# Performance work log

Hardware: AMD Instinct MI355X
Metric: run time of the kernel (lower is better)

The kernel has to match this reference:

```python
import jax, jax.numpy as jnp
import numpy as np

N = 1024
IN_FEATURES = 128
N_HEADS = 8
N_HIDDEN = 16  # out_features // n_heads = 128 // 8
NEG_SLOPE = 0.2


def setup_inputs() -> dict:
    key = jax.random.key(0)
    k1, k2, k3, k4, k5 = jax.random.split(key, 5)
    h = jax.random.normal(k1, (N, IN_FEATURES), dtype=jnp.float32)
    adj_mat = jax.random.randint(k2, (N, N, 1), 0, 2, dtype=jnp.int32)
    s = jax.random.normal(k3, (N, N, 1), dtype=jnp.float32)
    # linear: nn.Linear(in_features, n_hidden*n_heads, bias=False) -> weight [128, 128]
    W = jax.random.normal(k4, (N_HEADS * N_HIDDEN, IN_FEATURES), dtype=jnp.float32) * 0.1
    # attn: nn.Linear(2*n_hidden, 1, bias=False) -> weight [1, 32]; stored flat [32]
    attn_w = jax.random.normal(k5, (2 * N_HIDDEN,), dtype=jnp.float32) * 0.1
    return {"h": h, "adj_mat": adj_mat, "s": s, "W": W, "attn_w": attn_w}


def reference(h, adj_mat, s, W, attn_w):
    n_nodes = h.shape[0]
    # g: [N, heads, hidden]
    g = (h @ W.T).reshape(n_nodes, N_HEADS, N_HIDDEN)
    # attn(cat(g_i, g_j)) = a_src . g_i + a_dst . g_j  (linear decomposes over concat)
    a_src = attn_w[:N_HIDDEN]
    a_dst = attn_w[N_HIDDEN:]
    src = jnp.einsum('ihf,f->ih', g, a_src)  # [N, heads]
    dst = jnp.einsum('jhf,f->jh', g, a_dst)  # [N, heads]
    e = jax.nn.leaky_relu(src[:, None, :] + dst[None, :, :], NEG_SLOPE)  # [N, N, heads]
    mask = adj_mat == 0  # [N, N, 1] broadcasts over heads
    neg_inf = jnp.array(-jnp.inf, dtype=e.dtype)
    e = jnp.where(mask, neg_inf, e)
    s_masked = jnp.where(mask, neg_inf, s)  # [N, N, 1]
    a = jax.nn.softmax(e, axis=1)               # [N, N, heads]
    s_prime = jax.nn.softmax(s_masked, axis=1)  # [N, N, 1]
    # NOTE: original applies a third softmax to (a + s_prime) WITHOUT re-masking,
    # so non-edge entries (value 0) get nonzero weight exp(0)/Z — replicated faithfully.
    new_attention = jax.nn.softmax(a + s_prime, axis=1)  # [N, N, heads]
    # dropout is identity in eval mode
    attn_res = jnp.einsum('ijh,jhf->ihf', new_attention, g)  # [N, heads, hidden]
    return attn_res.reshape(n_nodes, N_HEADS * N_HIDDEN)
```

## Files before the change

### kernel.cpp

```cpp
#include <hip/hip_runtime.h>

#define NNODES 1024
#define NHEADS 8
#define NHID 16
#define DIM 128
#define NEG_SLOPE 0.2f

__global__ __launch_bounds__(128) void proj_kernel(
    const float* __restrict__ h, const float* __restrict__ W,
    const float* __restrict__ attn_w,
    float* __restrict__ g, float* __restrict__ srcv, float* __restrict__ dstv)
{
    const int i = blockIdx.x;
    const int o = threadIdx.x;
    __shared__ float hs[DIM];
    hs[o] = h[(size_t)i * DIM + o];
    __syncthreads();
    const float4* hv = (const float4*)hs;
    const float4* wv = (const float4*)(W + (size_t)o * DIM);
    float acc = 0.f;
#pragma unroll
    for (int k = 0; k < DIM / 4; k++) {
        float4 a = hv[k]; float4 b = wv[k];
        acc = fmaf(a.x, b.x, fmaf(a.y, b.y, fmaf(a.z, b.z, fmaf(a.w, b.w, acc))));
    }
    g[(size_t)i * DIM + o] = acc;
    const int f  = o & (NHID - 1);
    const int hd = o >> 4;
    float sv = acc * attn_w[f];
    float dv = acc * attn_w[NHID + f];
#pragma unroll
    for (int off = 8; off > 0; off >>= 1) {
        sv += __shfl_xor(sv, off, 64);
        dv += __shfl_xor(dv, off, 64);
    }
    if (f == 0) { srcv[i * NHEADS + hd] = sv; dstv[i * NHEADS + hd] = dv; }
}

__global__ __launch_bounds__(256, 2) void fused_kernel(
    const int* __restrict__ adj, const float* __restrict__ s,
    const float* __restrict__ g, const float* __restrict__ srcv,
    const float* __restrict__ dstv, float* __restrict__ out)
{
    const int i0   = blockIdx.x * 2;
    const int tid  = threadIdx.x;
    const int lane = tid & 63;
    const int wv   = tid >> 6;
    const int hA   = tid & 7;
    const int jsA  = tid >> 3;
    const int qB   = tid & 3;
    const int hB   = (tid >> 2) & 7;
    const int jsB  = tid >> 5;

    __shared__ float evL[2][NNODES];
    __shared__ float dstL[NNODES * NHEADS];
    __shared__ float sh_src[2][NHEADS];
    __shared__ float zeA[4][NHEADS][2];
    __shared__ float zsA[4][2];
    __shared__ float statE[2][NHEADS];
    __shared__ float statS[2];
    __shared__ float redO[4][2][NHEADS][4][4];
    __shared__ float ztA[4][2][NHEADS];

    float zs[2] = {0.f, 0.f};
#pragma unroll
    for (int r = 0; r < 2; r++) {
        const int4   a  = ((const int4*)  adj)[(size_t)(i0 + r) * (NNODES/4) + tid];
        const float4 sv = ((const float4*)s  )[(size_t)(i0 + r) * (NNODES/4) + tid];
        float4 e4;
        e4.x = a.x ? __expf(sv.x) : 0.f;
        e4.y = a.y ? __expf(sv.y) : 0.f;
        e4.z = a.z ? __expf(sv.z) : 0.f;
        e4.w = a.w ? __expf(sv.w) : 0.f;
        ((float4*)evL[r])[tid] = e4;
        zs[r] += e4.x + e4.y + e4.z + e4.w;
    }
    {
        const float4* dv4 = (const float4*)dstv;
        float4* dl4 = (float4*)dstL;
#pragma unroll
        for (int k = 0; k < 8; k++) dl4[k * 256 + tid] = dv4[k * 256 + tid];
        if (tid < 16) sh_src[tid >> 3][tid & 7] =
            srcv[(size_t)(i0 + (tid >> 3)) * NHEADS + (tid & 7)];
    }
    __syncthreads();

    float ze[2] = {0.f, 0.f};
    {
        const float sHA[2] = { sh_src[0][hA], sh_src[1][hA] };
#pragma unroll 4
        for (int t = 0; t < 32; t++) {
            const int j = t * 32 + jsA;
            const float d = dstL[j * NHEADS + hA];
#pragma unroll
            for (int r = 0; r < 2; r++) {
                float e = sHA[r] + d;
                e = e > 0.f ? e : NEG_SLOPE * e;
                const float x = __expf(e);
                ze[r] += (evL[r][j] != 0.f) ? x : 0.f;
            }
        }
    }
#pragma unroll
    for (int off = 8; off <= 32; off <<= 1)
#pragma unroll
        for (int r = 0; r < 2; r++) ze[r] += __shfl_xor(ze[r], off, 64);
#pragma unroll
    for (int off = 1; off <= 32; off <<= 1)
#pragma unroll
        for (int r = 0; r < 2; r++) zs[r] += __shfl_xor(zs[r], off, 64);
    if (lane < NHEADS) { zeA[wv][lane][0] = ze[0]; zeA[wv][lane][1] = ze[1]; }
    if (lane == 0)     { zsA[wv][0] = zs[0]; zsA[wv][1] = zs[1]; }
    __syncthreads();
    if (tid < 16) {
        const int hh = tid & 7, rr = tid >> 3;
        statE[rr][hh] = 1.f / (zeA[0][hh][rr] + zeA[1][hh][rr] +
                               zeA[2][hh][rr] + zeA[3][hh][rr]);
    } else if (tid < 18) {
        const int rr = tid - 16;
        statS[rr] = 1.f / (zsA[0][rr] + zsA[1][rr] + zsA[2][rr] + zsA[3][rr]);
    }
    __syncthreads();

    const float ize[2] = { statE[0][hB], statE[1][hB] };
    const float izs[2] = { statS[0],     statS[1]     };
    const float sHB[2] = { sh_src[0][hB], sh_src[1][hB] };
    const int   base   = lane & ~3;

    float acc[2][4] = {{0.f,0.f,0.f,0.f},{0.f,0.f,0.f,0.f}};
    float zt[2] = {0.f, 0.f};
    const float4* g4 = (const float4*)g;

#pragma unroll 2
    for (int tg = 0; tg < 32; tg++) {
        const int jw = (tg * 4 + qB) * 8 + jsB;
        const float d = dstL[jw * NHEADS + hB];
        float w[2];
#pragma unroll
        for (int r = 0; r < 2; r++) {
            float e = sHB[r] + d;
            e = e > 0.f ? e : NEG_SLOPE * e;
            const float x  = __expf(e);
            const float ev = evL[r][jw];
            const float arg = (ev != 0.f) ? fmaf(x, ize[r], ev * izs[r]) : 0.f;
            w[r] = __expf(arg);
            zt[r] += w[r];
        }
#pragma unroll
        for (int k = 0; k < 4; k++) {
            const int j = (tg * 4 + k) * 8 + jsB;
            const float4 gv = g4[(size_t)j * 32 + hB * 4 + qB];
            const float w0 = __shfl(w[0], base + k, 64);
            const float w1 = __shfl(w[1], base + k, 64);
            acc[0][0] = fmaf(w0, gv.x, acc[0][0]);
            acc[0][1] = fmaf(w0, gv.y, acc[0][1]);
            acc[0][2] = fmaf(w0, gv.z, acc[0][2]);
            acc[0][3] = fmaf(w0, gv.w, acc[0][3]);
            acc[1][0] = fmaf(w1, gv.x, acc[1][0]);
            acc[1][1] = fmaf(w1, gv.y, acc[1][1]);
            acc[1][2] = fmaf(w1, gv.z, acc[1][2]);
            acc[1][3] = fmaf(w1, gv.w, acc[1][3]);
        }
    }

#pragma unroll
    for (int r = 0; r < 2; r++)
#pragma unroll
        for (int m = 0; m < 4; m++) acc[r][m] += __shfl_xor(acc[r][m], 32, 64);
#pragma unroll
    for (int r = 0; r < 2; r++) {
        zt[r] += __shfl_xor(zt[r], 1, 64);
        zt[r] += __shfl_xor(zt[r], 2, 64);
        zt[r] += __shfl_xor(zt[r], 32, 64);
    }
    if (lane < 32) {
#pragma unroll
        for (int r = 0; r < 2; r++)
            *(float4*)&redO[wv][r][hB][qB][0] =
                make_float4(acc[r][0], acc[r][1], acc[r][2], acc[r][3]);
        if ((lane & 3) == 0) { ztA[wv][0][hB] = zt[0]; ztA[wv][1][hB] = zt[1]; }
    }
    __syncthreads();
    {
        const int rr = tid >> 7;
        const int hf = tid & 127;
        const int oh = hf >> 4;
        const int qq = (hf >> 2) & 3;
        const int mm = hf & 3;
        const float v  = redO[0][rr][oh][qq][mm] + redO[1][rr][oh][qq][mm] +
                         redO[2][rr][oh][qq][mm] + redO[3][rr][oh][qq][mm];
        const float zq = ztA[0][rr][oh] + ztA[1][rr][oh] +
                         ztA[2][rr][oh] + ztA[3][rr][oh];
        out[(size_t)(i0 + rr) * DIM + hf] = v / zq;
    }
}

extern "C" void kernel_launch(void* const* d_in, const int* in_sizes, int n_in,
                              void* d_out, int out_size, void* d_ws, size_t ws_size,
                              hipStream_t stream) {
    const float* h      = (const float*)d_in[0];
    const int*   adj    = (const int*)  d_in[1];
    const float* s      = (const float*)d_in[2];
    const float* W      = (const float*)d_in[3];
    const float* attn_w = (const float*)d_in[4];
    float* out = (float*)d_out;

    float* g    = (float*)d_ws;
    float* srcv = g    + (size_t)NNODES * DIM;
    float* dstv = srcv + (size_t)NNODES * NHEADS;

    proj_kernel <<<NNODES, DIM, 0, stream>>>(h, W, attn_w, g, srcv, dstv);
    fused_kernel<<<NNODES / 2, 256, 0, stream>>>(adj, s, g, srcv, dstv, out);
}
```

Before: 87.43 us.

## Store projected features in fp16 and cache first-pass exponentials in LDS

The projected feature matrix g is now written in half precision and read as packed half2 in the aggregation loop, which halves its memory traffic. The first pass stores exp(leaky_relu) values for both rows as half2 in a padded LDS buffer, so the second pass skips recomputing them, and dst values are read straight from global memory instead of being staged in LDS. The aggregation thread mapping changes so each thread owns 8 features and no cross-lane weight shuffles are needed. This cuts exp work and bandwidth but adds fp16 rounding error on g and the attention logits.

```diff
diff --git a/kernel.cpp b/kernel.cpp
--- a/kernel.cpp
+++ b/kernel.cpp
@@ -1,15 +1,19 @@
 #include <hip/hip_runtime.h>
+#include <hip/hip_fp16.h>
 
 #define NNODES 1024
 #define NHEADS 8
 #define NHID 16
 #define DIM 128
 #define NEG_SLOPE 0.2f
+#define XSTRIDE 36
+
+union F2H { float f; __half2 h; };
 
 __global__ __launch_bounds__(128) void proj_kernel(
     const float* __restrict__ h, const float* __restrict__ W,
     const float* __restrict__ attn_w,
-    float* __restrict__ g, float* __restrict__ srcv, float* __restrict__ dstv)
+    __half* __restrict__ gh, float* __restrict__ srcv, float* __restrict__ dstv)
 {
     const int i = blockIdx.x;
     const int o = threadIdx.x;
@@ -24,7 +28,7 @@
         float4 a = hv[k]; float4 b = wv[k];
         acc = fmaf(a.x, b.x, fmaf(a.y, b.y, fmaf(a.z, b.z, fmaf(a.w, b.w, acc))));
     }
-    g[(size_t)i * DIM + o] = acc;
+    gh[(size_t)i * DIM + o] = __float2half_rn(acc);
     const int f  = o & (NHID - 1);
     const int hd = o >> 4;
     float sv = acc * attn_w[f];
@@ -39,30 +43,25 @@
 
 __global__ __launch_bounds__(256, 2) void fused_kernel(
     const int* __restrict__ adj, const float* __restrict__ s,
-    const float* __restrict__ g, const float* __restrict__ srcv,
+    const __half* __restrict__ gh, const float* __restrict__ srcv,
     const float* __restrict__ dstv, float* __restrict__ out)
 {
     const int i0   = blockIdx.x * 2;
     const int tid  = threadIdx.x;
     const int lane = tid & 63;
     const int wv   = tid >> 6;
-    const int hA   = tid & 7;
-    const int jsA  = tid >> 3;
-    const int qB   = tid & 3;
-    const int hB   = (tid >> 2) & 7;
-    const int jsB  = tid >> 5;
 
     __shared__ float evL[2][NNODES];
-    __shared__ float dstL[NNODES * NHEADS];
+    __shared__ float xLf[256 * XSTRIDE];
     __shared__ float sh_src[2][NHEADS];
     __shared__ float zeA[4][NHEADS][2];
     __shared__ float zsA[4][2];
     __shared__ float statE[2][NHEADS];
     __shared__ float statS[2];
-    __shared__ float redO[4][2][NHEADS][4][4];
+    __shared__ float redO[4][2][NHEADS][2][8];
     __shared__ float ztA[4][2][NHEADS];
 
-    float zs[2] = {0.f, 0.f};
+    float zs0 = 0.f, zs1 = 0.f;
 #pragma unroll
     for (int r = 0; r < 2; r++) {
         const int4   a  = ((const int4*)  adj)[(size_t)(i0 + r) * (NNODES/4) + tid];
@@ -73,44 +72,55 @@
         e4.z = a.z ? __expf(sv.z) : 0.f;
         e4.w = a.w ? __expf(sv.w) : 0.f;
         ((float4*)evL[r])[tid] = e4;
-        zs[r] += e4.x + e4.y + e4.z + e4.w;
-    }
-    {
-        const float4* dv4 = (const float4*)dstv;
-        float4* dl4 = (float4*)dstL;
-#pragma unroll
-        for (int k = 0; k < 8; k++) dl4[k * 256 + tid] = dv4[k * 256 + tid];
-        if (tid < 16) sh_src[tid >> 3][tid & 7] =
-            srcv[(size_t)(i0 + (tid >> 3)) * NHEADS + (tid & 7)];
-    }
-    __syncthreads();
-
-    float ze[2] = {0.f, 0.f};
-    {
-        const float sHA[2] = { sh_src[0][hA], sh_src[1][hA] };
-#pragma unroll 4
-        for (int t = 0; t < 32; t++) {
-            const int j = t * 32 + jsA;
-            const float d = dstL[j * NHEADS + hA];
-#pragma unroll
-            for (int r = 0; r < 2; r++) {
-                float e = sHA[r] + d;
-                e = e > 0.f ? e : NEG_SLOPE * e;
-                const float x = __expf(e);
-                ze[r] += (evL[r][j] != 0.f) ? x : 0.f;
-            }
-        }
-    }
-#pragma unroll
-    for (int off = 8; off <= 32; off <<= 1)
-#pragma unroll
-        for (int r = 0; r < 2; r++) ze[r] += __shfl_xor(ze[r], off, 64);
-#pragma unroll
-    for (int off = 1; off <= 32; off <<= 1)
-#pragma unroll
-        for (int r = 0; r < 2; r++) zs[r] += __shfl_xor(zs[r], off, 64);
-    if (lane < NHEADS) { zeA[wv][lane][0] = ze[0]; zeA[wv][lane][1] = ze[1]; }
-    if (lane == 0)     { zsA[wv][0] = zs[0]; zsA[wv][1] = zs[1]; }
+        const float t = e4.x + e4.y + e4.z + e4.w;
+        if (r == 0) zs0 += t; else zs1 += t;
+    }
+    if (tid < 16) sh_src[tid >> 3][tid & 7] =
+        srcv[(size_t)(i0 + (tid >> 3)) * NHEADS + (tid & 7)];
+    __syncthreads();
+
+    const int hA = tid & 7;
+    const int jA = tid >> 3;
+    const float sA0 = sh_src[0][hA], sA1 = sh_src[1][hA];
+    float ze0 = 0.f, ze1 = 0.f;
+#pragma unroll 2
+    for (int t = 0; t < 8; t++) {
+        const int jg = t * 32 + jA;
+        const int j0 = jg * 4;
+        float dk[4];
+#pragma unroll
+        for (int k = 0; k < 4; k++) dk[k] = dstv[(size_t)(j0 + k) * NHEADS + hA];
+        const float4 e0q = *(const float4*)&evL[0][j0];
+        const float4 e1q = *(const float4*)&evL[1][j0];
+        const float ev0a[4] = {e0q.x, e0q.y, e0q.z, e0q.w};
+        const float ev1a[4] = {e1q.x, e1q.y, e1q.z, e1q.w};
+#pragma unroll
+        for (int k = 0; k < 4; k++) {
+            float e0 = sA0 + dk[k];
+            e0 = e0 > 0.f ? e0 : NEG_SLOPE * e0;
+            const float x0 = __expf(e0);
+            float e1 = sA1 + dk[k];
+            e1 = e1 > 0.f ? e1 : NEG_SLOPE * e1;
+            const float x1 = __expf(e1);
+            ze0 += (ev0a[k] != 0.f) ? x0 : 0.f;
+            ze1 += (ev1a[k] != 0.f) ? x1 : 0.f;
+            F2H u;
+            u.h = __halves2half2(__float2half_rn(x0), __float2half_rn(x1));
+            xLf[jg * XSTRIDE + hA * 4 + k] = u.f;
+        }
+    }
+#pragma unroll
+    for (int off = 8; off <= 32; off <<= 1) {
+        ze0 += __shfl_xor(ze0, off, 64);
+        ze1 += __shfl_xor(ze1, off, 64);
+    }
+#pragma unroll
+    for (int off = 1; off <= 32; off <<= 1) {
+        zs0 += __shfl_xor(zs0, off, 64);
+        zs1 += __shfl_xor(zs1, off, 64);
+    }
+    if (lane < NHEADS) { zeA[wv][lane][0] = ze0; zeA[wv][lane][1] = ze1; }
+    if (lane == 0)     { zsA[wv][0] = zs0; zsA[wv][1] = zs1; }
     __syncthreads();
     if (tid < 16) {
         const int hh = tid & 7, rr = tid >> 3;
@@ -122,73 +132,87 @@
     }
     __syncthreads();
 
-    const float ize[2] = { statE[0][hB], statE[1][hB] };
-    const float izs[2] = { statS[0],     statS[1]     };
-    const float sHB[2] = { sh_src[0][hB], sh_src[1][hB] };
-    const int   base   = lane & ~3;
-
-    float acc[2][4] = {{0.f,0.f,0.f,0.f},{0.f,0.f,0.f,0.f}};
-    float zt[2] = {0.f, 0.f};
-    const float4* g4 = (const float4*)g;
+    const int q1  = tid & 1;
+    const int hB  = (tid >> 1) & 7;
+    const int jsB = tid >> 4;
+    const int fbase = hB * NHID + q1 * 8;
+    const float ize0 = statE[0][hB], ize1 = statE[1][hB];
+    const float izs0 = statS[0],     izs1 = statS[1];
+
+    float acc0[8], acc1[8];
+#pragma unroll
+    for (int m = 0; m < 8; m++) { acc0[m] = 0.f; acc1[m] = 0.f; }
+    float zt0 = 0.f, zt1 = 0.f;
 
 #pragma unroll 2
-    for (int tg = 0; tg < 32; tg++) {
-        const int jw = (tg * 4 + qB) * 8 + jsB;
-        const float d = dstL[jw * NHEADS + hB];
-        float w[2];
-#pragma unroll
-        for (int r = 0; r < 2; r++) {
-            float e = sHB[r] + d;
-            e = e > 0.f ? e : NEG_SLOPE * e;
-            const float x  = __expf(e);
-            const float ev = evL[r][jw];
-            const float arg = (ev != 0.f) ? fmaf(x, ize[r], ev * izs[r]) : 0.f;
-            w[r] = __expf(arg);
-            zt[r] += w[r];
-        }
+    for (int tg = 0; tg < 16; tg++) {
+        const int jg = tg * 16 + jsB;
+        const int j0 = jg * 4;
+        const float4 xq  = *(const float4*)&xLf[jg * XSTRIDE + hB * 4];
+        const float4 e0q = *(const float4*)&evL[0][j0];
+        const float4 e1q = *(const float4*)&evL[1][j0];
+        const float xa[4]   = {xq.x, xq.y, xq.z, xq.w};
+        const float ev0a[4] = {e0q.x, e0q.y, e0q.z, e0q.w};
+        const float ev1a[4] = {e1q.x, e1q.y, e1q.z, e1q.w};
 #pragma unroll
         for (int k = 0; k < 4; k++) {
-            const int j = (tg * 4 + k) * 8 + jsB;
-            const float4 gv = g4[(size_t)j * 32 + hB * 4 + qB];
-            const float w0 = __shfl(w[0], base + k, 64);
-            const float w1 = __shfl(w[1], base + k, 64);
-            acc[0][0] = fmaf(w0, gv.x, acc[0][0]);
-            acc[0][1] = fmaf(w0, gv.y, acc[0][1]);
-            acc[0][2] = fmaf(w0, gv.z, acc[0][2]);
-            acc[0][3] = fmaf(w0, gv.w, acc[0][3]);
-            acc[1][0] = fmaf(w1, gv.x, acc[1][0]);
-            acc[1][1] = fmaf(w1, gv.y, acc[1][1]);
-            acc[1][2] = fmaf(w1, gv.z, acc[1][2]);
-            acc[1][3] = fmaf(w1, gv.w, acc[1][3]);
-        }
-    }
-
-#pragma unroll
-    for (int r = 0; r < 2; r++)
-#pragma unroll
-        for (int m = 0; m < 4; m++) acc[r][m] += __shfl_xor(acc[r][m], 32, 64);
-#pragma unroll
-    for (int r = 0; r < 2; r++) {
-        zt[r] += __shfl_xor(zt[r], 1, 64);
-        zt[r] += __shfl_xor(zt[r], 2, 64);
-        zt[r] += __shfl_xor(zt[r], 32, 64);
-    }
-    if (lane < 32) {
-#pragma unroll
-        for (int r = 0; r < 2; r++)
-            *(float4*)&redO[wv][r][hB][qB][0] =
-                make_float4(acc[r][0], acc[r][1], acc[r][2], acc[r][3]);
-        if ((lane & 3) == 0) { ztA[wv][0][hB] = zt[0]; ztA[wv][1][hB] = zt[1]; }
+            F2H u; u.f = xa[k];
+            const float x0 = __low2float(u.h);
+            const float x1 = __high2float(u.h);
+            const float ev0 = ev0a[k], ev1 = ev1a[k];
+            const float a0 = (ev0 != 0.f) ? fmaf(x0, ize0, ev0 * izs0) : 0.f;
+            const float a1 = (ev1 != 0.f) ? fmaf(x1, ize1, ev1 * izs1) : 0.f;
+            const float w0 = __expf(a0);
+            const float w1 = __expf(a1);
+            zt0 += w0; zt1 += w1;
+            const float4 gv = *(const float4*)(gh + (size_t)(j0 + k) * DIM + fbase);
+            F2H g0, g1, g2, g3;
+            g0.f = gv.x; g1.f = gv.y; g2.f = gv.z; g3.f = gv.w;
+            const float2 p0 = __half22float2(g0.h);
+            const float2 p1 = __half22float2(g1.h);
+            const float2 p2 = __half22float2(g2.h);
+            const float2 p3 = __half22float2(g3.h);
+            acc0[0] = fmaf(w0, p0.x, acc0[0]); acc1[0] = fmaf(w1, p0.x, acc1[0]);
+            acc0[1] = fmaf(w0, p0.y, acc0[1]); acc1[1] = fmaf(w1, p0.y, acc1[1]);
+            acc0[2] = fmaf(w0, p1.x, acc0[2]); acc1[2] = fmaf(w1, p1.x, acc1[2]);
+            acc0[3] = fmaf(w0, p1.y, acc0[3]); acc1[3] = fmaf(w1, p1.y, acc1[3]);
+            acc0[4] = fmaf(w0, p2.x, acc0[4]); acc1[4] = fmaf(w1, p2.x, acc1[4]);
+            acc0[5] = fmaf(w0, p2.y, acc0[5]); acc1[5] = fmaf(w1, p2.y, acc1[5]);
+            acc0[6] = fmaf(w0, p3.x, acc0[6]); acc1[6] = fmaf(w1, p3.x, acc1[6]);
+            acc0[7] = fmaf(w0, p3.y, acc0[7]); acc1[7] = fmaf(w1, p3.y, acc1[7]);
+        }
+    }
+
+#pragma unroll
+    for (int off = 16; off <= 32; off <<= 1) {
+#pragma unroll
+        for (int m = 0; m < 8; m++) {
+            acc0[m] += __shfl_xor(acc0[m], off, 64);
+            acc1[m] += __shfl_xor(acc1[m], off, 64);
+        }
+        zt0 += __shfl_xor(zt0, off, 64);
+        zt1 += __shfl_xor(zt1, off, 64);
+    }
+    if (lane < 16) {
+#pragma unroll
+        for (int m = 0; m < 8; m++) {
+            redO[wv][0][hB][q1][m] = acc0[m];
+            redO[wv][1][hB][q1][m] = acc1[m];
+        }
+    }
+    if ((lane & 0x31) == 0) {
+        ztA[wv][0][hB] = zt0;
+        ztA[wv][1][hB] = zt1;
     }
     __syncthreads();
     {
         const int rr = tid >> 7;
         const int hf = tid & 127;
         const int oh = hf >> 4;
-        const int qq = (hf >> 2) & 3;
-        const int mm = hf & 3;
-        const float v  = redO[0][rr][oh][qq][mm] + redO[1][rr][oh][qq][mm] +
-                         redO[2][rr][oh][qq][mm] + redO[3][rr][oh][qq][mm];
+        const int qq = (hf >> 3) & 1;
+        const int f8 = hf & 7;
+        const float v  = redO[0][rr][oh][qq][f8] + redO[1][rr][oh][qq][f8] +
+                         redO[2][rr][oh][qq][f8] + redO[3][rr][oh][qq][f8];
         const float zq = ztA[0][rr][oh] + ztA[1][rr][oh] +
                          ztA[2][rr][oh] + ztA[3][rr][oh];
         out[(size_t)(i0 + rr) * DIM + hf] = v / zq;
@@ -205,10 +229,10 @@
     const float* attn_w = (const float*)d_in[4];
     float* out = (float*)d_out;
 
-    float* g    = (float*)d_ws;
-    float* srcv = g    + (size_t)NNODES * DIM;
-    float* dstv = srcv + (size_t)NNODES * NHEADS;
-
-    proj_kernel <<<NNODES, DIM, 0, stream>>>(h, W, attn_w, g, srcv, dstv);
-    fused_kernel<<<NNODES / 2, 256, 0, stream>>>(adj, s, g, srcv, dstv, out);
+    __half* gh   = (__half*)d_ws;
+    float*  srcv = (float*)((char*)d_ws + (size_t)NNODES * DIM * sizeof(__half));
+    float*  dstv = srcv + (size_t)NNODES * NHEADS;
+
+    proj_kernel <<<NNODES, DIM, 0, stream>>>(h, W, attn_w, gh, srcv, dstv);
+    fused_kernel<<<NNODES / 2, 256, 0, stream>>>(adj, s, gh, srcv, dstv, out);
 }
```

After: 87.46 us. No clear change (+0.0%).
